# Kernel tuning notes

Measured on AMD Instinct MI355X. Metric: run time of the kernel, lower is better.

## Reference

```python
import jax, jax.numpy as jnp
import numpy as np
import math

B, T, D = 4, 4096, 512   # batch, seq, n_embd
E, K, H = 4, 2, 4 * 512  # num_experts, top_experts, expert hidden


def gelu_gpt2(x):
    # 0.5*x*(1+tanh(sqrt(2/pi)*(x+0.044715*x^3)))
    c = math.sqrt(2.0 / math.pi)
    return 0.5 * x * (1.0 + jnp.tanh(c * (x + 0.044715 * x ** 3)))


def setup_inputs() -> dict:
    key = jax.random.key(0)
    ks = jax.random.split(key, 5)
    s = 0.02
    return {
        "x": jax.random.normal(ks[0], (B, T, D), dtype=jnp.float32),
        "gate_w": (jax.random.normal(ks[1], (E, D)) * s).astype(jnp.float32),  # nn.Linear weight [out,in]
        "w1": (jax.random.normal(ks[2], (E, H, D)) * s).astype(jnp.float32),
        "b1": jnp.zeros((E, H), dtype=jnp.float32),
        "w2": (jax.random.normal(ks[3], (E, D, H)) * s).astype(jnp.float32),
        "b2": jnp.zeros((E, D), dtype=jnp.float32),
    }


def reference(x, gate_w, w1, b1, w2, b2):
    d = x.shape[-1]
    xf = x.reshape(-1, d)                              # [N, D]
    gate = xf @ gate_w.T                               # [N, E]
    # load_balancing_loss: torch.mean over dims (0,1) of a 2D tensor -> scalar
    m = jnp.mean(gate)
    balancing_loss = jnp.sum(m * jnp.log(m + 0.1))
    # top-k routing + softmax over selected logits (computed in fp32)
    w, idx = jax.lax.top_k(gate, K)                    # [N, K]
    w = jax.nn.softmax(w.astype(jnp.float32), axis=1).astype(x.dtype)
    # dense combine weights [N, E]; zero for unselected experts -> identical math
    cw = jnp.sum(jax.nn.one_hot(idx, E, dtype=x.dtype) * w[..., None], axis=1)
    # run every expert on every token, weighted combine (dropout = eval identity)
    h = jnp.einsum('nd,ehd->neh', xf, w1) + b1         # [N, E, H]
    h = gelu_gpt2(h)
    o = jnp.einsum('neh,edh->ned', h, w2) + b2         # [N, E, D]
    out = jnp.einsum('ned,ne->nd', o, cw)              # [N, D]
    return out.reshape(x.shape), balancing_loss
```

## Files before the change

kernel.cpp:

```cpp
#include <hip/hip_runtime.h>
#include <hip/hip_bf16.h>
#include <cmath>
#include <cstdint>

#define N_TOK 16384
#define DIM   512
#define HID   2048
#define NEXP  4
#define MAX_WL 260

typedef __attribute__((ext_vector_type(8))) short bf16x8;
typedef __attribute__((ext_vector_type(4))) float f32x4;

__device__ __forceinline__ short f2bf(float f) {
  __hip_bfloat16 h = __float2bfloat16(f);
  return *reinterpret_cast<short*>(&h);
}

__device__ __forceinline__ float gelu_f(float v) {
  float v2 = v * v;
  float u = v * (1.5957691216057308f + 0.07135481283254937f * v2);
  return v / (1.0f + __expf(-u));
}

__device__ __forceinline__ void load_lds16(const void* g, void* l) {
  __builtin_amdgcn_global_load_lds(
      (const __attribute__((address_space(1))) void*)g,
      (__attribute__((address_space(3))) void*)l, 16, 0, 0);
}

#define LDSIDX(r, c16) (((r) * 64) + ((((c16) ^ ((r) & 7)) * 8)))

__global__ void cvt_kernel(const float* __restrict__ src, short* __restrict__ dst, int n4) {
  int i = blockIdx.x * blockDim.x + threadIdx.x;
  int stride = gridDim.x * blockDim.x;
  for (; i < n4; i += stride) {
    float4 v = reinterpret_cast<const float4*>(src)[i];
    short4 o;
    o.x = f2bf(v.x); o.y = f2bf(v.y); o.z = f2bf(v.z); o.w = f2bf(v.w);
    reinterpret_cast<short4*>(dst)[i] = o;
  }
}

__global__ __launch_bounds__(256) void gate_kernel(
    const float* __restrict__ x, const float* __restrict__ gw,
    float* __restrict__ cw, float* __restrict__ gate_sum,
    short* __restrict__ xb) {
  int t = threadIdx.x, wid = t >> 6, lane = t & 63;

  float4 g[NEXP][2];
#pragma unroll
  for (int e = 0; e < NEXP; ++e) {
    const float4* gp = reinterpret_cast<const float4*>(gw + e * DIM + lane * 8);
    g[e][0] = gp[0]; g[e][1] = gp[1];
  }

  float lsum = 0.0f;
  int n0 = blockIdx.x * 64 + wid * 16;
  for (int i = 0; i < 16; ++i) {
    int n = n0 + i;
    const float4* xr4 = reinterpret_cast<const float4*>(x + (size_t)n * DIM);
    float4 a = xr4[lane * 2];
    float4 b = xr4[lane * 2 + 1];

    short4 s0, s1;
    s0.x = f2bf(a.x); s0.y = f2bf(a.y); s0.z = f2bf(a.z); s0.w = f2bf(a.w);
    s1.x = f2bf(b.x); s1.y = f2bf(b.y); s1.z = f2bf(b.z); s1.w = f2bf(b.w);
    short4* xbp = reinterpret_cast<short4*>(xb + (size_t)n * DIM + lane * 8);
    xbp[0] = s0; xbp[1] = s1;

    float p[NEXP];
#pragma unroll
    for (int e = 0; e < NEXP; ++e) {
      p[e] = a.x * g[e][0].x + a.y * g[e][0].y + a.z * g[e][0].z + a.w * g[e][0].w
           + b.x * g[e][1].x + b.y * g[e][1].y + b.z * g[e][1].z + b.w * g[e][1].w;
    }
#pragma unroll
    for (int e = 0; e < NEXP; ++e)
#pragma unroll
      for (int off = 32; off; off >>= 1) p[e] += __shfl_xor(p[e], off);

    if (lane == 0) {
      lsum += p[0] + p[1] + p[2] + p[3];
      int i0 = 0;
#pragma unroll
      for (int e = 1; e < NEXP; ++e) if (p[e] > p[i0]) i0 = e;
      int i1 = -1;
#pragma unroll
      for (int e = 0; e < NEXP; ++e) {
        if (e == i0) continue;
        if (i1 < 0 || p[e] > p[i1]) i1 = e;
      }
      float eb = expf(p[i1] - p[i0]);
      float w0 = 1.0f / (1.0f + eb);
      float w1 = eb / (1.0f + eb);
      float row[NEXP] = {0.f, 0.f, 0.f, 0.f};
      row[i0] = w0; row[i1] = w1;
#pragma unroll
      for (int e = 0; e < NEXP; ++e) cw[n * NEXP + e] = row[e];
    }
  }
  __shared__ float bs[4];
  if (lane == 0) bs[wid] = lsum;
  __syncthreads();
  if (t == 0) atomicAdd(gate_sum, bs[0] + bs[1] + bs[2] + bs[3]);
}

__global__ void loss_kernel(const float* __restrict__ gate_sum, float* __restrict__ out_loss) {
  float m = gate_sum[0] / (float)(N_TOK * NEXP);
  out_loss[0] = m * logf(m + 0.1f);
}

__global__ __launch_bounds__(256) void count_kernel(const float* __restrict__ cw,
                                                    int* __restrict__ blockcnt) {
  __shared__ int c[4];
  int t = threadIdx.x;
  if (t < 4) c[t] = 0;
  __syncthreads();
  int n = blockIdx.x * 256 + t;
  float4 w = reinterpret_cast<const float4*>(cw)[n];
  unsigned long long m0 = __ballot(w.x != 0.f);
  unsigned long long m1 = __ballot(w.y != 0.f);
  unsigned long long m2 = __ballot(w.z != 0.f);
  unsigned long long m3 = __ballot(w.w != 0.f);
  if ((t & 63) == 0) {
    atomicAdd(&c[0], (int)__popcll(m0));
    atomicAdd(&c[1], (int)__popcll(m1));
    atomicAdd(&c[2], (int)__popcll(m2));
    atomicAdd(&c[3], (int)__popcll(m3));
  }
  __syncthreads();
  if (t < 4) blockcnt[blockIdx.x * 4 + t] = c[t];
}

__global__ void scan_kernel(const int* __restrict__ blockcnt, int* __restrict__ blockoff,
                            int* __restrict__ counts, int* __restrict__ expbase,
                            int* __restrict__ wl, int* __restrict__ wl_n) {
  int lane = threadIdx.x;
  int tot[NEXP];
#pragma unroll
  for (int e = 0; e < NEXP; ++e) {
    int v = blockcnt[lane * 4 + e];
    int inc = v;
#pragma unroll
    for (int off = 1; off < 64; off <<= 1) {
      int u = __shfl_up(inc, off);
      if (lane >= off) inc += u;
    }
    blockoff[lane * 4 + e] = inc - v;
    tot[e] = __shfl(inc, 63);
  }
  if (lane == 0) {
    int base = 0;
#pragma unroll
    for (int e = 0; e < NEXP; ++e) {
      counts[e] = tot[e];
      expbase[e] = base;
      base += tot[e];
    }
    int n = 0;
    for (int e = 0; e < NEXP; ++e) {
      int nb = (tot[e] + 127) >> 7;
      for (int b = 0; b < nb; ++b) wl[n++] = (e << 20) | b;
    }
    wl_n[0] = n;
  }
}

__global__ __launch_bounds__(256) void write_kernel(const float* __restrict__ cw,
                                                    const int* __restrict__ blockoff,
                                                    const int* __restrict__ expbase,
                                                    int* __restrict__ list) {
  int t = threadIdx.x, wave = t >> 6, lane = t & 63;
  int blk = blockIdx.x;
  int n = blk * 256 + t;
  float4 w4 = reinterpret_cast<const float4*>(cw)[n];
  float wf[4] = {w4.x, w4.y, w4.z, w4.w};
  __shared__ int wcnt[4][4];
  unsigned long long lt = (1ULL << lane) - 1ULL;
  int pfx[4]; bool sel[4];
#pragma unroll
  for (int e = 0; e < NEXP; ++e) {
    sel[e] = (wf[e] != 0.f);
    unsigned long long m = __ballot(sel[e]);
    pfx[e] = (int)__popcll(m & lt);
    if (lane == 0) wcnt[wave][e] = (int)__popcll(m);
  }
  __syncthreads();
#pragma unroll
  for (int e = 0; e < NEXP; ++e) {
    if (sel[e]) {
      int woff = 0;
      for (int w2 = 0; w2 < wave; ++w2) woff += wcnt[w2][e];
      list[expbase[e] + blockoff[blk * 4 + e] + woff + pfx[e]] = n;
    }
  }
}

__global__ __launch_bounds__(256) void moe_gemm1(
    const short* __restrict__ xb, const short* __restrict__ w1b,
    const float* __restrict__ b1, short* __restrict__ Hc,
    const int* __restrict__ list, const int* __restrict__ counts,
    const int* __restrict__ expbase, const int* __restrict__ wl,
    const int* __restrict__ wl_n) {
  int lg = ((blockIdx.x & 7) * (MAX_WL * 2)) + (blockIdx.x >> 3);
  int bn = lg & 15, widx = lg >> 4;
  if (widx >= wl_n[0]) return;
  int entry = wl[widx];
  int e = entry >> 20, bm = entry & 0xFFFFF;
  int cnt = counts[e];
  int base = expbase[e];
  int bm0 = bm * 128;
  int bn0 = bn * 128;
  const short* Bw = w1b + (size_t)e * HID * DIM;

  int t = threadIdx.x, lane = t & 63, wid = t >> 6;
  int srow = t >> 3;
  int scol = ((t & 7) ^ (srow & 7)) * 8;
  const short* Ag[4];
#pragma unroll
  for (int i = 0; i < 4; ++i) {
    int rc = bm0 + i * 32 + srow;
    int tok = list[base + ((rc < cnt) ? rc : 0)];
    Ag[i] = xb + (size_t)tok * DIM + scol;
  }
  const short* Bg = Bw + (size_t)(bn0 + srow) * DIM + scol;

  __shared__ __align__(16) short As[128 * 64];
  __shared__ __align__(16) short Bs[128 * 64];
  f32x4 acc[4][4] = {};
  int wr = (wid >> 1) * 64, wc = (wid & 1) * 64;

  for (int kt = 0; kt < DIM / 64; ++kt) {
    if (kt) __syncthreads();
    int k0 = kt * 64;
#pragma unroll
    for (int i = 0; i < 4; ++i) {
      load_lds16(Ag[i] + k0, As + i * 2048 + t * 8);
      load_lds16(Bg + (size_t)(i * 32) * DIM + k0, Bs + i * 2048 + t * 8);
    }
    __syncthreads();
#pragma unroll
    for (int ks = 0; ks < 2; ++ks) {
      bf16x8 af[4], bfr[4];
#pragma unroll
      for (int mi = 0; mi < 4; ++mi) {
        int r = wr + mi * 16 + (lane & 15);
        af[mi] = *(const bf16x8*)&As[LDSIDX(r, ks * 4 + (lane >> 4))];
      }
#pragma unroll
      for (int ni = 0; ni < 4; ++ni) {
        int r = wc + ni * 16 + (lane & 15);
        bfr[ni] = *(const bf16x8*)&Bs[LDSIDX(r, ks * 4 + (lane >> 4))];
      }
#pragma unroll
      for (int mi = 0; mi < 4; ++mi)
#pragma unroll
        for (int ni = 0; ni < 4; ++ni)
          acc[mi][ni] = __builtin_amdgcn_mfma_f32_16x16x32_bf16(af[mi], bfr[ni], acc[mi][ni], 0, 0, 0);
    }
  }

  int crow = (lane >> 4) * 4, ccol = lane & 15;
#pragma unroll
  for (int mi = 0; mi < 4; ++mi) {
#pragma unroll
    for (int ni = 0; ni < 4; ++ni) {
      int col = bn0 + wc + ni * 16 + ccol;
      float bv = b1[(size_t)e * HID + col];
#pragma unroll
      for (int j = 0; j < 4; ++j) {
        int rc = bm0 + wr + mi * 16 + crow + j;
        if (rc < cnt)
          Hc[(size_t)(base + rc) * HID + col] = f2bf(gelu_f(acc[mi][ni][j] + bv));
      }
    }
  }
}

__global__ __launch_bounds__(256) void moe_gemm2(
    const short* __restrict__ Hc, const short* __restrict__ w2b,
    const float* __restrict__ b2, float* __restrict__ out,
    const float* __restrict__ cw, const int* __restrict__ list,
    const int* __restrict__ counts, const int* __restrict__ expbase,
    const int* __restrict__ wl, const int* __restrict__ wl_n) {
  int lg = ((blockIdx.x & 7) * (MAX_WL / 2)) + (blockIdx.x >> 3);
  int bn = lg & 3, widx = lg >> 2;
  if (widx >= wl_n[0]) return;
  int entry = wl[widx];
  int e = entry >> 20, bm = entry & 0xFFFFF;
  int cnt = counts[e];
  int base = expbase[e];
  int bm0 = bm * 128;
  int bn0 = bn * 128;
  const short* Bw = w2b + (size_t)e * DIM * HID;

  int t = threadIdx.x, lane = t & 63, wid = t >> 6;
  int srow = t >> 3;
  int scol = ((t & 7) ^ (srow & 7)) * 8;
  const short* Ag = Hc + (size_t)(base + bm0 + srow) * HID + scol;
  const short* Bg = Bw + (size_t)(bn0 + srow) * HID + scol;

  __shared__ __align__(16) short As[128 * 64];
  __shared__ __align__(16) short Bs[128 * 64];
  f32x4 acc[4][4] = {};
  int wr = (wid >> 1) * 64, wc = (wid & 1) * 64;

  for (int kt = 0; kt < HID / 64; ++kt) {
    if (kt) __syncthreads();
    int k0 = kt * 64;
#pragma unroll
    for (int i = 0; i < 4; ++i) {
      load_lds16(Ag + (size_t)(i * 32) * HID + k0, As + i * 2048 + t * 8);
      load_lds16(Bg + (size_t)(i * 32) * HID + k0, Bs + i * 2048 + t * 8);
    }
    __syncthreads();
#pragma unroll
    for (int ks = 0; ks < 2; ++ks) {
      bf16x8 af[4], bfr[4];
#pragma unroll
      for (int mi = 0; mi < 4; ++mi) {
        int r = wr + mi * 16 + (lane & 15);
        af[mi] = *(const bf16x8*)&As[LDSIDX(r, ks * 4 + (lane >> 4))];
      }
#pragma unroll
      for (int ni = 0; ni < 4; ++ni) {
        int r = wc + ni * 16 + (lane & 15);
        bfr[ni] = *(const bf16x8*)&Bs[LDSIDX(r, ks * 4 + (lane >> 4))];
      }
#pragma unroll
      for (int mi = 0; mi < 4; ++mi)
#pragma unroll
        for (int ni = 0; ni < 4; ++ni)
          acc[mi][ni] = __builtin_amdgcn_mfma_f32_16x16x32_bf16(af[mi], bfr[ni], acc[mi][ni], 0, 0, 0);
    }
  }

  int crow = (lane >> 4) * 4, ccol = lane & 15;
#pragma unroll
  for (int mi = 0; mi < 4; ++mi) {
    int tokr[4]; float wgtr[4]; bool val[4];
#pragma unroll
    for (int j = 0; j < 4; ++j) {
      int rc = bm0 + wr + mi * 16 + crow + j;
      val[j] = (rc < cnt);
      int tok = list[base + (val[j] ? rc : 0)];
      tokr[j] = tok;
      wgtr[j] = cw[tok * NEXP + e];
    }
#pragma unroll
    for (int ni = 0; ni < 4; ++ni) {
      int col = bn0 + wc + ni * 16 + ccol;
      float bv = b2[(size_t)e * DIM + col];
#pragma unroll
      for (int j = 0; j < 4; ++j) {
        if (val[j])
          atomicAdd(&out[(size_t)tokr[j] * DIM + col], wgtr[j] * (acc[mi][ni][j] + bv));
      }
    }
  }
}

template <int KDIM, int EPI>
__global__ __launch_bounds__(256) void gemm_kernel(
    const short* __restrict__ A, const short* __restrict__ B,
    const float* __restrict__ bias,
    short* __restrict__ Hout, float* __restrict__ out,
    const float* __restrict__ cw, int expert) {
  constexpr int BK = 64;
  __shared__ __align__(16) short As[128 * BK];
  __shared__ __align__(16) short Bs[128 * BK];
  int t = threadIdx.x;
  int lane = t & 63, wid = t >> 6;
  int bn0 = blockIdx.x * 128;
  int bm0 = blockIdx.y * 128;
  int wr = (wid >> 1) * 64;
  int wc = (wid & 1) * 64;
  f32x4 acc[4][4] = {};
  int srow = t >> 3;
  int scol = (t & 7) * 8;
  const short* Ag = A + (size_t)(bm0 + srow) * KDIM + scol;
  const short* Bg = B + (size_t)(bn0 + srow) * KDIM + scol;
  for (int kt = 0; kt < KDIM / BK; ++kt) {
    if (kt) __syncthreads();
    int k0 = kt * BK;
#pragma unroll
    for (int i = 0; i < 4; ++i) {
      load_lds16(Ag + (size_t)(i * 32) * KDIM + k0, As + i * 2048 + t * 8);
      load_lds16(Bg + (size_t)(i * 32) * KDIM + k0, Bs + i * 2048 + t * 8);
    }
    __syncthreads();
#pragma unroll
    for (int ks = 0; ks < 2; ++ks) {
      int koff = ks * 32 + ((lane >> 4) << 3);
      bf16x8 af[4], bfr[4];
#pragma unroll
      for (int mi = 0; mi < 4; ++mi)
        af[mi] = *(const bf16x8*)&As[(wr + mi * 16 + (lane & 15)) * BK + koff];
#pragma unroll
      for (int ni = 0; ni < 4; ++ni)
        bfr[ni] = *(const bf16x8*)&Bs[(wc + ni * 16 + (lane & 15)) * BK + koff];
#pragma unroll
      for (int mi = 0; mi < 4; ++mi)
#pragma unroll
        for (int ni = 0; ni < 4; ++ni)
          acc[mi][ni] = __builtin_amdgcn_mfma_f32_16x16x32_bf16(af[mi], bfr[ni], acc[mi][ni], 0, 0, 0);
    }
  }
  int crow = (lane >> 4) * 4;
  int ccol = lane & 15;
#pragma unroll
  for (int mi = 0; mi < 4; ++mi) {
#pragma unroll
    for (int ni = 0; ni < 4; ++ni) {
      int col = bn0 + wc + ni * 16 + ccol;
      float bv = bias[col];
#pragma unroll
      for (int j = 0; j < 4; ++j) {
        int row = bm0 + wr + mi * 16 + crow + j;
        float v = acc[mi][ni][j] + bv;
        if constexpr (EPI == 0) {
          Hout[(size_t)row * HID + col] = f2bf(gelu_f(v));
        } else {
          float w = cw[row * NEXP + expert];
          float r = w * v;
          if constexpr (EPI == 1) out[(size_t)row * DIM + col] = r;
          else                    out[(size_t)row * DIM + col] += r;
        }
      }
    }
  }
}

extern "C" void kernel_launch(void* const* d_in, const int* in_sizes, int n_in,
                              void* d_out, int out_size, void* d_ws, size_t ws_size,
                              hipStream_t stream) {
  const float* x  = (const float*)d_in[0];
  const float* gw = (const float*)d_in[1];
  const float* w1 = (const float*)d_in[2];
  const float* b1 = (const float*)d_in[3];
  const float* w2 = (const float*)d_in[4];
  const float* b2 = (const float*)d_in[5];
  float* out = (float*)d_out;

  char* ws = (char*)d_ws;
  float* cw       = (float*)(ws + 0);
  float* gate_sum = (float*)(ws + 262144);
  int*   blockcnt = (int*)(ws + 262400);
  int*   blockoff = (int*)(ws + 263424);
  int*   counts   = (int*)(ws + 264448);
  int*   expbase  = (int*)(ws + 264512);
  int*   wl_n     = (int*)(ws + 264576);
  int*   wl       = (int*)(ws + 264640);
  int*   list     = (int*)(ws + 266176);
  short* xb       = (short*)(ws + 397248);
  short* w1b      = (short*)(ws + 17174464);
  short* w2b      = (short*)(ws + 25563072);
  short* Hc       = (short*)(ws + 33951680);
  const size_t ROUTED_NEED = 33951680ull + (size_t)(32768 + 128) * HID * 2;

  hipMemsetAsync(gate_sum, 0, sizeof(float), stream);
  cvt_kernel<<<1024, 256, 0, stream>>>(w1, w1b, NEXP * HID * DIM / 4);
  cvt_kernel<<<1024, 256, 0, stream>>>(w2, w2b, NEXP * DIM * HID / 4);
  gate_kernel<<<N_TOK / 64, 256, 0, stream>>>(x, gw, cw, gate_sum, xb);
  loss_kernel<<<1, 1, 0, stream>>>(gate_sum, out + (size_t)N_TOK * DIM);

  if (ws_size >= ROUTED_NEED) {
    hipMemsetAsync(out, 0, (size_t)N_TOK * DIM * sizeof(float), stream);
    count_kernel<<<64, 256, 0, stream>>>(cw, blockcnt);
    scan_kernel<<<1, 64, 0, stream>>>(blockcnt, blockoff, counts, expbase, wl, wl_n);
    write_kernel<<<64, 256, 0, stream>>>(cw, blockoff, expbase, list);
    moe_gemm1<<<MAX_WL * 16, 256, 0, stream>>>(
        xb, w1b, b1, Hc, list, counts, expbase, wl, wl_n);
    moe_gemm2<<<MAX_WL * 4, 256, 0, stream>>>(
        Hc, w2b, b2, out, cw, list, counts, expbase, wl, wl_n);
  } else {
    short* Hb = (short*)(ws + 33816832);
    for (int e = 0; e < NEXP; ++e) {
      gemm_kernel<DIM, 0><<<dim3(HID / 128, N_TOK / 128), 256, 0, stream>>>(
          xb, w1b + (size_t)e * HID * DIM, b1 + (size_t)e * HID, Hb, nullptr, nullptr, e);
      if (e == 0)
        gemm_kernel<HID, 1><<<dim3(DIM / 128, N_TOK / 128), 256, 0, stream>>>(
            Hb, w2b + (size_t)e * DIM * HID, b2 + (size_t)e * DIM, nullptr, out, cw, e);
      else
        gemm_kernel<HID, 2><<<dim3(DIM / 128, N_TOK / 128), 256, 0, stream>>>(
            Hb, w2b + (size_t)e * DIM * HID, b2 + (size_t)e * DIM, nullptr, out, cw, e);
    }
  }
}
```

Baseline: 431.7 us.

## Double-buffer LDS tiles in both expert GEMM kernels

Both expert GEMM kernels now allocate two LDS buffers for the A and B tiles. The loads for the next K tile are issued into the spare buffer before the MFMAs on the current tile run, which removes one barrier per iteration and lets global-to-LDS loads overlap compute. LDS use per block doubles to 64KB, which can lower occupancy. The barrier placement relies on load_lds16 completion semantics at __syncthreads.

```diff
diff --git a/kernel.cpp b/kernel.cpp
--- a/kernel.cpp
+++ b/kernel.cpp
@@ -226,32 +226,43 @@
   }
   const short* Bg = Bw + (size_t)(bn0 + srow) * DIM + scol;
 
-  __shared__ __align__(16) short As[128 * 64];
-  __shared__ __align__(16) short Bs[128 * 64];
+  __shared__ __align__(16) short As[2][128 * 64];
+  __shared__ __align__(16) short Bs[2][128 * 64];
   f32x4 acc[4][4] = {};
   int wr = (wid >> 1) * 64, wc = (wid & 1) * 64;
-
-  for (int kt = 0; kt < DIM / 64; ++kt) {
-    if (kt) __syncthreads();
-    int k0 = kt * 64;
-#pragma unroll
-    for (int i = 0; i < 4; ++i) {
-      load_lds16(Ag[i] + k0, As + i * 2048 + t * 8);
-      load_lds16(Bg + (size_t)(i * 32) * DIM + k0, Bs + i * 2048 + t * 8);
-    }
-    __syncthreads();
+  constexpr int NT = DIM / 64;
+
+#pragma unroll
+  for (int i = 0; i < 4; ++i) {
+    load_lds16(Ag[i], As[0] + i * 2048 + t * 8);
+    load_lds16(Bg + (size_t)(i * 32) * DIM, Bs[0] + i * 2048 + t * 8);
+  }
+  __syncthreads();
+
+  int cur = 0;
+  for (int kt = 0; kt < NT; ++kt) {
+    if (kt + 1 < NT) {
+      int k0n = (kt + 1) * 64;
+#pragma unroll
+      for (int i = 0; i < 4; ++i) {
+        load_lds16(Ag[i] + k0n, As[cur ^ 1] + i * 2048 + t * 8);
+        load_lds16(Bg + (size_t)(i * 32) * DIM + k0n, Bs[cur ^ 1] + i * 2048 + t * 8);
+      }
+    }
+    const short* Asb = As[cur];
+    const short* Bsb = Bs[cur];
 #pragma unroll
     for (int ks = 0; ks < 2; ++ks) {
       bf16x8 af[4], bfr[4];
 #pragma unroll
       for (int mi = 0; mi < 4; ++mi) {
         int r = wr + mi * 16 + (lane & 15);
-        af[mi] = *(const bf16x8*)&As[LDSIDX(r, ks * 4 + (lane >> 4))];
+        af[mi] = *(const bf16x8*)&Asb[LDSIDX(r, ks * 4 + (lane >> 4))];
       }
 #pragma unroll
       for (int ni = 0; ni < 4; ++ni) {
         int r = wc + ni * 16 + (lane & 15);
-        bfr[ni] = *(const bf16x8*)&Bs[LDSIDX(r, ks * 4 + (lane >> 4))];
+        bfr[ni] = *(const bf16x8*)&Bsb[LDSIDX(r, ks * 4 + (lane >> 4))];
       }
 #pragma unroll
       for (int mi = 0; mi < 4; ++mi)
@@ -259,6 +270,8 @@
         for (int ni = 0; ni < 4; ++ni)
           acc[mi][ni] = __builtin_amdgcn_mfma_f32_16x16x32_bf16(af[mi], bfr[ni], acc[mi][ni], 0, 0, 0);
     }
+    __syncthreads();
+    cur ^= 1;
   }
 
   int crow = (lane >> 4) * 4, ccol = lane & 15;
@@ -301,32 +314,43 @@
   const short* Ag = Hc + (size_t)(base + bm0 + srow) * HID + scol;
   const short* Bg = Bw + (size_t)(bn0 + srow) * HID + scol;
 
-  __shared__ __align__(16) short As[128 * 64];
-  __shared__ __align__(16) short Bs[128 * 64];
+  __shared__ __align__(16) short As[2][128 * 64];
+  __shared__ __align__(16) short Bs[2][128 * 64];
   f32x4 acc[4][4] = {};
   int wr = (wid >> 1) * 64, wc = (wid & 1) * 64;
-
-  for (int kt = 0; kt < HID / 64; ++kt) {
-    if (kt) __syncthreads();
-    int k0 = kt * 64;
-#pragma unroll
-    for (int i = 0; i < 4; ++i) {
-      load_lds16(Ag + (size_t)(i * 32) * HID + k0, As + i * 2048 + t * 8);
-      load_lds16(Bg + (size_t)(i * 32) * HID + k0, Bs + i * 2048 + t * 8);
-    }
-    __syncthreads();
+  constexpr int NT = HID / 64;
+
+#pragma unroll
+  for (int i = 0; i < 4; ++i) {
+    load_lds16(Ag + (size_t)(i * 32) * HID, As[0] + i * 2048 + t * 8);
+    load_lds16(Bg + (size_t)(i * 32) * HID, Bs[0] + i * 2048 + t * 8);
+  }
+  __syncthreads();
+
+  int cur = 0;
+  for (int kt = 0; kt < NT; ++kt) {
+    if (kt + 1 < NT) {
+      int k0n = (kt + 1) * 64;
+#pragma unroll
+      for (int i = 0; i < 4; ++i) {
+        load_lds16(Ag + (size_t)(i * 32) * HID + k0n, As[cur ^ 1] + i * 2048 + t * 8);
+        load_lds16(Bg + (size_t)(i * 32) * HID + k0n, Bs[cur ^ 1] + i * 2048 + t * 8);
+      }
+    }
+    const short* Asb = As[cur];
+    const short* Bsb = Bs[cur];
 #pragma unroll
     for (int ks = 0; ks < 2; ++ks) {
       bf16x8 af[4], bfr[4];
 #pragma unroll
       for (int mi = 0; mi < 4; ++mi) {
         int r = wr + mi * 16 + (lane & 15);
-        af[mi] = *(const bf16x8*)&As[LDSIDX(r, ks * 4 + (lane >> 4))];
+        af[mi] = *(const bf16x8*)&Asb[LDSIDX(r, ks * 4 + (lane >> 4))];
       }
 #pragma unroll
       for (int ni = 0; ni < 4; ++ni) {
         int r = wc + ni * 16 + (lane & 15);
-        bfr[ni] = *(const bf16x8*)&Bs[LDSIDX(r, ks * 4 + (lane >> 4))];
+        bfr[ni] = *(const bf16x8*)&Bsb[LDSIDX(r, ks * 4 + (lane >> 4))];
       }
 #pragma unroll
       for (int mi = 0; mi < 4; ++mi)
@@ -334,6 +358,8 @@
         for (int ni = 0; ni < 4; ++ni)
           acc[mi][ni] = __builtin_amdgcn_mfma_f32_16x16x32_bf16(af[mi], bfr[ni], acc[mi][ni], 0, 0, 0);
     }
+    __syncthreads();
+    cur ^= 1;
   }
 
   int crow = (lane >> 4) * 4, ccol = lane & 15;
```

Measured after the change: 521.3 us. 1.21x slower.

## Replace atomic scatter in expert GEMM2 with compact output and gather combine

Applied to the files above, without the earlier changes.

Expert GEMM2 now writes per-slot results (with bias) to a compact fp32 buffer instead of atomically adding weighted rows into the output. The routing write kernel also records each token's two slot positions. A new combine kernel gathers the two rows and applies the routing weights. This removes the output memset and the global atomics, at the cost of a larger workspace, an extra kernel, and extra round-trip memory traffic. The path is enabled only when the workspace is big enough.

```diff
diff --git a/kernel.cpp b/kernel.cpp
--- a/kernel.cpp
+++ b/kernel.cpp
@@ -170,7 +170,8 @@
 __global__ __launch_bounds__(256) void write_kernel(const float* __restrict__ cw,
                                                     const int* __restrict__ blockoff,
                                                     const int* __restrict__ expbase,
-                                                    int* __restrict__ list) {
+                                                    int* __restrict__ list,
+                                                    int* __restrict__ inv) {
   int t = threadIdx.x, wave = t >> 6, lane = t & 63;
   int blk = blockIdx.x;
   int n = blk * 256 + t;
@@ -187,12 +188,16 @@
     if (lane == 0) wcnt[wave][e] = (int)__popcll(m);
   }
   __syncthreads();
+  int kk = 0;
 #pragma unroll
   for (int e = 0; e < NEXP; ++e) {
     if (sel[e]) {
       int woff = 0;
       for (int w2 = 0; w2 < wave; ++w2) woff += wcnt[w2][e];
-      list[expbase[e] + blockoff[blk * 4 + e] + woff + pfx[e]] = n;
+      int pos = expbase[e] + blockoff[blk * 4 + e] + woff + pfx[e];
+      list[pos] = n;
+      inv[n * 2 + kk] = pos | (e << 20);
+      ++kk;
     }
   }
 }
@@ -281,9 +286,10 @@
 __global__ __launch_bounds__(256) void moe_gemm2(
     const short* __restrict__ Hc, const short* __restrict__ w2b,
     const float* __restrict__ b2, float* __restrict__ out,
-    const float* __restrict__ cw, const int* __restrict__ list,
-    const int* __restrict__ counts, const int* __restrict__ expbase,
-    const int* __restrict__ wl, const int* __restrict__ wl_n) {
+    float* __restrict__ Oc, const float* __restrict__ cw,
+    const int* __restrict__ list, const int* __restrict__ counts,
+    const int* __restrict__ expbase, const int* __restrict__ wl,
+    const int* __restrict__ wl_n, int use_compact) {
   int lg = ((blockIdx.x & 7) * (MAX_WL / 2)) + (blockIdx.x >> 3);
   int bn = lg & 3, widx = lg >> 2;
   if (widx >= wl_n[0]) return;
@@ -337,28 +343,67 @@
   }
 
   int crow = (lane >> 4) * 4, ccol = lane & 15;
-#pragma unroll
-  for (int mi = 0; mi < 4; ++mi) {
-    int tokr[4]; float wgtr[4]; bool val[4];
-#pragma unroll
-    for (int j = 0; j < 4; ++j) {
-      int rc = bm0 + wr + mi * 16 + crow + j;
-      val[j] = (rc < cnt);
-      int tok = list[base + (val[j] ? rc : 0)];
-      tokr[j] = tok;
-      wgtr[j] = cw[tok * NEXP + e];
-    }
-#pragma unroll
-    for (int ni = 0; ni < 4; ++ni) {
-      int col = bn0 + wc + ni * 16 + ccol;
-      float bv = b2[(size_t)e * DIM + col];
+  if (use_compact) {
+#pragma unroll
+    for (int mi = 0; mi < 4; ++mi) {
+#pragma unroll
+      for (int ni = 0; ni < 4; ++ni) {
+        int col = bn0 + wc + ni * 16 + ccol;
+        float bv = b2[(size_t)e * DIM + col];
+#pragma unroll
+        for (int j = 0; j < 4; ++j) {
+          int rc = bm0 + wr + mi * 16 + crow + j;
+          if (rc < cnt)
+            Oc[(size_t)(base + rc) * DIM + col] = acc[mi][ni][j] + bv;
+        }
+      }
+    }
+  } else {
+#pragma unroll
+    for (int mi = 0; mi < 4; ++mi) {
+      int tokr[4]; float wgtr[4]; bool val[4];
 #pragma unroll
       for (int j = 0; j < 4; ++j) {
-        if (val[j])
-          atomicAdd(&out[(size_t)tokr[j] * DIM + col], wgtr[j] * (acc[mi][ni][j] + bv));
-      }
-    }
-  }
+        int rc = bm0 + wr + mi * 16 + crow + j;
+        val[j] = (rc < cnt);
+        int tok = list[base + (val[j] ? rc : 0)];
+        tokr[j] = tok;
+        wgtr[j] = cw[tok * NEXP + e];
+      }
+#pragma unroll
+      for (int ni = 0; ni < 4; ++ni) {
+        int col = bn0 + wc + ni * 16 + ccol;
+        float bv = b2[(size_t)e * DIM + col];
+#pragma unroll
+        for (int j = 0; j < 4; ++j) {
+          if (val[j])
+            atomicAdd(&out[(size_t)tokr[j] * DIM + col], wgtr[j] * (acc[mi][ni][j] + bv));
+        }
+      }
+    }
+  }
+}
+
+__global__ __launch_bounds__(256) void combine_kernel(
+    const float* __restrict__ Oc, const int* __restrict__ inv,
+    const float* __restrict__ cw, float* __restrict__ out) {
+  int i = blockIdx.x * 256 + threadIdx.x;
+  int n = i >> 7;
+  int c4 = i & 127;
+  int v0 = inv[n * 2], v1 = inv[n * 2 + 1];
+  int p0 = v0 & 0xFFFFF, e0 = v0 >> 20;
+  int p1 = v1 & 0xFFFFF, e1 = v1 >> 20;
+  float w0 = cw[n * NEXP + e0];
+  float w1 = cw[n * NEXP + e1];
+  const float4* O4 = reinterpret_cast<const float4*>(Oc);
+  float4 a = O4[(size_t)p0 * 128 + c4];
+  float4 b = O4[(size_t)p1 * 128 + c4];
+  float4 o;
+  o.x = w0 * a.x + w1 * b.x;
+  o.y = w0 * a.y + w1 * b.y;
+  o.z = w0 * a.z + w1 * b.z;
+  o.w = w0 * a.w + w1 * b.w;
+  reinterpret_cast<float4*>(out)[i] = o;
 }
 
 template <int KDIM, int EPI>
@@ -453,11 +498,15 @@
   int*   wl_n     = (int*)(ws + 264576);
   int*   wl       = (int*)(ws + 264640);
   int*   list     = (int*)(ws + 266176);
-  short* xb       = (short*)(ws + 397248);
-  short* w1b      = (short*)(ws + 17174464);
-  short* w2b      = (short*)(ws + 25563072);
-  short* Hc       = (short*)(ws + 33951680);
-  const size_t ROUTED_NEED = 33951680ull + (size_t)(32768 + 128) * HID * 2;
+  int*   inv      = (int*)(ws + 397248);
+  short* xb       = (short*)(ws + 528320);
+  short* w1b      = (short*)(ws + 17305536);
+  short* w2b      = (short*)(ws + 25694144);
+  short* Hc       = (short*)(ws + 34082752);
+  float* Oc       = (float*)(ws + 168824768);
+  const size_t ROUTED_NEED  = 168824768ull;
+  const size_t COMPACT_NEED = 236195776ull;
+  int use_compact = (ws_size >= COMPACT_NEED) ? 1 : 0;
 
   hipMemsetAsync(gate_sum, 0, sizeof(float), stream);
   cvt_kernel<<<1024, 256, 0, stream>>>(w1, w1b, NEXP * HID * DIM / 4);
@@ -466,14 +515,17 @@
   loss_kernel<<<1, 1, 0, stream>>>(gate_sum, out + (size_t)N_TOK * DIM);
 
   if (ws_size >= ROUTED_NEED) {
-    hipMemsetAsync(out, 0, (size_t)N_TOK * DIM * sizeof(float), stream);
+    if (!use_compact)
+      hipMemsetAsync(out, 0, (size_t)N_TOK * DIM * sizeof(float), stream);
     count_kernel<<<64, 256, 0, stream>>>(cw, blockcnt);
     scan_kernel<<<1, 64, 0, stream>>>(blockcnt, blockoff, counts, expbase, wl, wl_n);
-    write_kernel<<<64, 256, 0, stream>>>(cw, blockoff, expbase, list);
+    write_kernel<<<64, 256, 0, stream>>>(cw, blockoff, expbase, list, inv);
     moe_gemm1<<<MAX_WL * 16, 256, 0, stream>>>(
         xb, w1b, b1, Hc, list, counts, expbase, wl, wl_n);
     moe_gemm2<<<MAX_WL * 4, 256, 0, stream>>>(
-        Hc, w2b, b2, out, cw, list, counts, expbase, wl, wl_n);
+        Hc, w2b, b2, out, Oc, cw, list, counts, expbase, wl, wl_n, use_compact);
+    if (use_compact)
+      combine_kernel<<<N_TOK * DIM / 4 / 256, 256, 0, stream>>>(Oc, inv, cw, out);
   } else {
     short* Hb = (short*)(ws + 33816832);
     for (int e = 0; e < NEXP; ++e) {
```

Result: faster. 410.0 us (-5.0%).
